# Optimization experiments

Hardware: AMD Instinct MI355X
Metric: run time of the kernel (lower is better)

The kernel has to match this reference:

```python
import jax, jax.numpy as jnp
import numpy as np

B, S, H, R = 32, 1024, 768, 24
ATT_EPS = 1e10
LN_EPS = 1e-12


def setup_inputs() -> dict:
    key = jax.random.key(0)
    ks = jax.random.split(key, 20)
    sc = 0.02
    inp = {
        "relation": jax.random.randint(ks[0], (B, 1), 0, R),
        "last_hidden_size": jax.random.normal(ks[1], (B, S, H), dtype=jnp.float32),
        "sub_head": jax.random.randint(ks[2], (B, 1), 0, S),
        "sub_tail": jax.random.randint(ks[3], (B, 1), 0, S),
        "attention_mask": jnp.ones((B, S), dtype=jnp.float32),
        # learned parameters
        "rel_emb": jax.random.normal(ks[4], (R, H)) * sc,
        "W_rf": jax.random.normal(ks[5], (H, H)) * sc,
        "b_rf": jnp.zeros((H,), jnp.float32),
        "gamma": jnp.ones((H,), jnp.float32),
        "beta": jnp.zeros((H,), jnp.float32),
        "W_wd": jax.random.normal(ks[6], (H, 2 * H)) * sc,
        "W_bd": jax.random.normal(ks[7], (H, 2 * H)) * sc,
        "Wq": jax.random.normal(ks[8], (H, H)) * sc,
        "bq": jnp.zeros((H,), jnp.float32),
        "Wk": jax.random.normal(ks[9], (H, H)) * sc,
        "bk": jnp.zeros((H,), jnp.float32),
        "Wv": jax.random.normal(ks[10], (H, H)) * sc,
        "bv": jnp.zeros((H,), jnp.float32),
        "W_obj": jax.random.normal(ks[11], (1, H)) * sc,
        "b_obj": jnp.zeros((1,), jnp.float32),
    }
    return inp


def reference(relation, last_hidden_size, sub_head, sub_tail, attention_mask,
              rel_emb, W_rf, b_rf, gamma, beta, W_wd, W_bd,
              Wq, bq, Wk, bk, Wv, bv, W_obj, b_obj):
    # dropout layers are identity in eval mode
    # relation feature: embedding -> linear -> ReLU6   [B,1,H]
    rel_feature = jnp.clip(rel_emb[relation] @ W_rf.T + b_rf, 0.0, 6.0)
    # subject span features via gather                 [B,1,H]
    sh = jnp.take_along_axis(last_hidden_size, sub_head[:, :, None], axis=1)
    st = jnp.take_along_axis(last_hidden_size, sub_tail[:, :, None], axis=1)
    sub_feature = (sh + st) * 0.5
    cond = jnp.concatenate([rel_feature, sub_feature], axis=-1)  # [B,1,2H]

    # conditional layer norm: per-sample affine from condition
    weight = cond @ W_wd.T + gamma  # [B,1,H]
    bias = cond @ W_bd.T + beta     # [B,1,H]
    mean = jnp.mean(last_hidden_size, axis=-1, keepdims=True)
    ctr = last_hidden_size - mean
    var = jnp.mean(ctr * ctr, axis=-1, keepdims=True)
    x = ctr / jnp.sqrt(var + LN_EPS)
    x = x * weight + bias  # [B,S,H]

    # custom attention: ReLU-activated q/k/v, additive mask bias, residual
    q = jax.nn.relu(x @ Wq.T + bq)
    k = jax.nn.relu(x @ Wk.T + bk)
    v = jax.nn.relu(x @ Wv.T + bv)
    e = jnp.einsum('bsh,bth->bst', q, k)  # [B,S,S]
    e = e - ATT_EPS * (1.0 - attention_mask[:, None, :])
    a = jax.nn.softmax(e, axis=-1)
    hidden = jnp.einsum('bst,bth->bsh', a, v) + x  # residual

    pred_obj_head = jnp.squeeze(hidden @ W_obj.T + b_obj, axis=-1)  # [B,S]
    return pred_obj_head, hidden
```

## Files before the change

### kernel.cpp

```cpp
#include <hip/hip_runtime.h>

constexpr int NB  = 32;
constexpr int NS  = 1024;
constexpr int NH  = 768;
constexpr int NH2 = 1536;
constexpr int NQKV = 2304;
constexpr int NBS = NB * NS;

typedef __bf16 bf16x8 __attribute__((ext_vector_type(8)));
typedef float  f32x4  __attribute__((ext_vector_type(4)));
typedef unsigned short u16x8 __attribute__((ext_vector_type(8)));

__device__ __forceinline__ unsigned short f2bf(float f) {
  unsigned int u = __builtin_bit_cast(unsigned int, f);
  u += 0x7FFFu + ((u >> 16) & 1u);
  return (unsigned short)(u >> 16);
}
__device__ __forceinline__ float bf2f(unsigned short h) {
  return __builtin_bit_cast(float, ((unsigned int)h) << 16);
}

#define GLDS16(g, l)                                                         \
  __builtin_amdgcn_global_load_lds(                                          \
      (__attribute__((address_space(1))) void*)(g),                          \
      (__attribute__((address_space(3))) void*)(l), 16, 0, 0)

#define SBAR()   asm volatile("s_barrier" ::: "memory")
#define WAITVM8() asm volatile("s_waitcnt vmcnt(8)" ::: "memory")
#define WAITVM0() asm volatile("s_waitcnt vmcnt(0)" ::: "memory")

__launch_bounds__(256)
__global__ void cond_pre(const int* __restrict__ relation,
                         const float* __restrict__ h,
                         const int* __restrict__ subh,
                         const int* __restrict__ subt,
                         const float* __restrict__ rel_emb,
                         float* __restrict__ reT, float* __restrict__ condT) {
  const int b = blockIdx.x, t = threadIdx.x;
  const int r = relation[b], sh = subh[b], st = subt[b];
  for (int k = t; k < NH; k += 256) {
    reT[(size_t)k * NB + b] = rel_emb[(size_t)r * NH + k];
    condT[(size_t)(NH + k) * NB + b] =
        0.5f * (h[((size_t)b * NS + sh) * NH + k] +
                h[((size_t)b * NS + st) * NH + k]);
  }
}

__launch_bounds__(256)
__global__ void cond_rf(const float* __restrict__ W_rf,
                        const float* __restrict__ b_rf,
                        const float* __restrict__ reT,
                        float* __restrict__ condT) {
  const int t = threadIdx.x;
  const int b = t & 31, jl = t >> 5;
  const int j = blockIdx.x * 8 + jl;
  const float4* w4 = (const float4*)(W_rf + (size_t)j * NH);
  const float* rT = reT + b;
  float a0 = 0.f, a1 = 0.f;
  for (int k4 = 0; k4 < NH / 4; k4++) {
    float4 w = w4[k4];
    const float* c = rT + (size_t)(k4 * 4) * NB;
    a0 += w.x * c[0] + w.y * c[NB];
    a1 += w.z * c[2 * NB] + w.w * c[3 * NB];
  }
  float acc = a0 + a1 + b_rf[j];
  condT[(size_t)j * NB + b] = fminf(fmaxf(acc, 0.0f), 6.0f);
}

__launch_bounds__(256)
__global__ void cond_wb(const float* __restrict__ W_wd,
                        const float* __restrict__ W_bd,
                        const float* __restrict__ gamma,
                        const float* __restrict__ beta,
                        const float* __restrict__ condT,
                        float* __restrict__ wt, float* __restrict__ bs) {
  __shared__ float redW[128], redB[128];
  const int t = threadIdx.x;
  const int b = t & 31, jl = (t >> 5) & 3, ks = t >> 7;
  const int j = blockIdx.x * 4 + jl;
  const float4* ww = (const float4*)(W_wd + (size_t)j * NH2 + ks * NH);
  const float4* wb = (const float4*)(W_bd + (size_t)j * NH2 + ks * NH);
  const float* cT = condT + (size_t)ks * NH * NB + b;
  float aw0 = 0.f, aw1 = 0.f, ab0 = 0.f, ab1 = 0.f;
  for (int k4 = 0; k4 < NH / 4; k4++) {
    float4 w = ww[k4];
    float4 v = wb[k4];
    const float* c = cT + (size_t)(k4 * 4) * NB;
    float c0 = c[0], c1 = c[NB], c2 = c[2 * NB], c3 = c[3 * NB];
    aw0 += w.x * c0 + w.y * c1;
    aw1 += w.z * c2 + w.w * c3;
    ab0 += v.x * c0 + v.y * c1;
    ab1 += v.z * c2 + v.w * c3;
  }
  float aw = aw0 + aw1, ab = ab0 + ab1;
  if (ks == 1) {
    redW[t - 128] = aw;
    redB[t - 128] = ab;
  }
  __syncthreads();
  if (ks == 0) {
    aw += redW[t];
    ab += redB[t];
    wt[(size_t)b * NH + j] = aw + gamma[j];
    bs[(size_t)b * NH + j] = ab + beta[j];
  }
}

__launch_bounds__(64)
__global__ void ln_kernel(const float* __restrict__ h,
                          const float* __restrict__ wt,
                          const float* __restrict__ bs,
                          unsigned short* __restrict__ xbf) {
  const int row = blockIdx.x;
  const int b = row >> 10;
  const int lane = threadIdx.x;
  const float4* hr = (const float4*)(h + (size_t)row * NH);
  float4 v0 = hr[lane], v1 = hr[lane + 64], v2 = hr[lane + 128];
  float sum = 0.f, sq = 0.f;
  {
    sum += v0.x + v0.y + v0.z + v0.w;
    sq  += v0.x * v0.x + v0.y * v0.y + v0.z * v0.z + v0.w * v0.w;
    sum += v1.x + v1.y + v1.z + v1.w;
    sq  += v1.x * v1.x + v1.y * v1.y + v1.z * v1.z + v1.w * v1.w;
    sum += v2.x + v2.y + v2.z + v2.w;
    sq  += v2.x * v2.x + v2.y * v2.y + v2.z * v2.z + v2.w * v2.w;
  }
  for (int off = 32; off > 0; off >>= 1) {
    sum += __shfl_xor(sum, off, 64);
    sq  += __shfl_xor(sq, off, 64);
  }
  const float mean = sum * (1.0f / NH);
  const float var  = sq * (1.0f / NH) - mean * mean;
  const float rstd = rsqrtf(var + 1e-12f);
  const float4* wr = (const float4*)(wt + (size_t)b * NH);
  const float4* br = (const float4*)(bs + (size_t)b * NH);
  ushort4* xr = (ushort4*)(xbf + (size_t)row * NH);
#pragma unroll
  for (int i = 0; i < 3; i++) {
    float4 v = (i == 0) ? v0 : (i == 1) ? v1 : v2;
    float4 w = wr[lane + 64 * i];
    float4 bb = br[lane + 64 * i];
    ushort4 o;
    o.x = f2bf((v.x - mean) * rstd * w.x + bb.x);
    o.y = f2bf((v.y - mean) * rstd * w.y + bb.y);
    o.z = f2bf((v.z - mean) * rstd * w.z + bb.z);
    o.w = f2bf((v.w - mean) * rstd * w.w + bb.w);
    xr[lane + 64 * i] = o;
  }
}

__launch_bounds__(256)
__global__ void prep_w(const float* __restrict__ Wq, const float* __restrict__ bq,
                       const float* __restrict__ Wk, const float* __restrict__ bk,
                       const float* __restrict__ Wv, const float* __restrict__ bv,
                       unsigned short* __restrict__ Wcat, float* __restrict__ bcat) {
  const int row = blockIdx.x;
  const float* Wsrc;
  const float* bsrc;
  int r;
  if (row < NH) { Wsrc = Wq; bsrc = bq; r = row; }
  else if (row < NH2) { Wsrc = Wk; bsrc = bk; r = row - NH; }
  else { Wsrc = Wv; bsrc = bv; r = row - NH2; }
  for (int j = threadIdx.x; j < NH; j += 256)
    Wcat[(size_t)row * NH + j] = f2bf(Wsrc[(size_t)r * NH + j]);
  if (threadIdx.x == 0) bcat[row] = bsrc[r];
}

template <int OUT_BF16, int RELU, int HASBIAS, int RES>
__launch_bounds__(512, 2)
__global__ void gemm256(const unsigned short* __restrict__ A, long long sAz, int lda,
                        const unsigned short* __restrict__ Bm, long long sBz, int ldb,
                        void* __restrict__ C, long long sCz, int ldc,
                        const float* __restrict__ bias,
                        const unsigned short* __restrict__ Res, long long sRz, int ldr,
                        int K, int doswz) {
  extern __shared__ char lds[];
  const int t = threadIdx.x;
  const int z = blockIdx.z;
  int id = blockIdx.x + blockIdx.y * gridDim.x;
  if (doswz) {
    const int cpx = (gridDim.x * gridDim.y) >> 3;
    id = (id & 7) * cpx + (id >> 3);
  }
  const int tileN = (id % gridDim.x) * 256;
  const int tileM = (id / gridDim.x) * 256;
  const unsigned short* Ab = A + (size_t)z * sAz + (size_t)tileM * lda;
  const unsigned short* Bb = Bm + (size_t)z * sBz + (size_t)tileN * ldb;

  const int lane = t & 63;
  const int w = t >> 6;
  const int wm = w >> 2, wn = w & 3;
  const int lr = lane & 15, hi = lane >> 4;
  const int swz = (lane & 7) << 4;
  char* myA = lds + wm * 16384;
  char* myB = lds + 65536 + (wn >> 1) * 16384;
  const int rb0 = (wn & 1) * 64;

  const int sr = t >> 3;
  const int scc = (t & 7) ^ (sr & 7);

#define STAGE(Gb, ld, dst)                                                  \
  do {                                                                      \
    _Pragma("unroll") for (int hl_ = 0; hl_ < 4; hl_++) {                   \
      GLDS16((Gb) + (size_t)(hl_ * 64 + sr) * (ld) + scc * 8,               \
             (dst) + hl_ * 8192 + (size_t)t * 16);                          \
    }                                                                       \
  } while (0)

  f32x4 acc[8][4];
#pragma unroll
  for (int m = 0; m < 8; m++)
#pragma unroll
    for (int n = 0; n < 4; n++) acc[m][n] = (f32x4)0.0f;

  const int NT = K >> 6;

  STAGE(Ab, lda, lds);
  STAGE(Bb, ldb, lds + 65536);
  STAGE(Ab + 64, lda, lds + 32768);
  STAGE(Bb + 64, ldb, lds + 65536 + 32768);
  WAITVM8();
  SBAR();

  for (int kt = 0; kt < NT; kt++) {
    const int bb = kt & 1;
    const char* Ah = myA + bb * 32768;
    const char* Bh = myB + bb * 32768;
#pragma unroll
    for (int ks = 0; ks < 2; ks++) {
      const int cb = (ks * 64 + hi * 16) ^ swz;
      bf16x8 af[8], bfr[4];
#pragma unroll
      for (int m = 0; m < 8; m++)
        af[m] = *(const bf16x8*)(Ah + (m * 16 + lr) * 128 + cb);
#pragma unroll
      for (int n = 0; n < 4; n++)
        bfr[n] = *(const bf16x8*)(Bh + (rb0 + n * 16 + lr) * 128 + cb);
      __builtin_amdgcn_s_setprio(1);
#pragma unroll
      for (int m = 0; m < 8; m++)
#pragma unroll
        for (int n = 0; n < 4; n++)
          acc[m][n] = __builtin_amdgcn_mfma_f32_16x16x32_bf16(af[m], bfr[n],
                                                              acc[m][n], 0, 0, 0);
      __builtin_amdgcn_s_setprio(0);
    }
    if (kt == NT - 1) break;
    SBAR();
    if (kt + 2 < NT) {
      STAGE(Ab + (kt + 2) * 64, lda, lds + bb * 32768);
      STAGE(Bb + (kt + 2) * 64, ldb, lds + 65536 + bb * 32768);
      WAITVM8();
    } else {
      WAITVM0();
    }
    SBAR();
  }

  const int row0 = tileM + wm * 128;
  const int col0 = tileN + wn * 64;
#pragma unroll
  for (int m = 0; m < 8; m++) {
    const int rowb = row0 + m * 16 + hi * 4;
#pragma unroll
    for (int n = 0; n < 4; n++) {
      const int col = col0 + n * 16 + lr;
      const float bv = HASBIAS ? bias[col] : 0.0f;
      f32x4 v = acc[m][n];
#pragma unroll
      for (int r = 0; r < 4; r++) {
        float x = v[r] + bv;
        if (RELU) x = fmaxf(x, 0.0f);
        if (RES)
          x += bf2f(Res[(size_t)z * sRz + (size_t)(rowb + r) * ldr + col]);
        if (OUT_BF16)
          ((unsigned short*)C)[(size_t)z * sCz + (size_t)(rowb + r) * ldc + col] =
              f2bf(x);
        else
          ((float*)C)[(size_t)z * sCz + (size_t)(rowb + r) * ldc + col] = x;
      }
    }
  }
#undef STAGE
}

__launch_bounds__(256)
__global__ void softmax_kernel(float* __restrict__ e,
                               const float* __restrict__ mask, int b0) {
  const int ri = blockIdx.x;
  const int lb = blockIdx.y;
  const int b = b0 + lb;
  float* row = e + ((size_t)lb * NS + ri) * NS;
  const int t = threadIdx.x;
  float4 v = ((const float4*)row)[t];
  float4 m = ((const float4*)(mask + (size_t)b * NS))[t];
  v.x -= 1e10f * (1.0f - m.x);
  v.y -= 1e10f * (1.0f - m.y);
  v.z -= 1e10f * (1.0f - m.z);
  v.w -= 1e10f * (1.0f - m.w);
  float mx = fmaxf(fmaxf(v.x, v.y), fmaxf(v.z, v.w));
  __shared__ float red[4];
  for (int off = 32; off > 0; off >>= 1) mx = fmaxf(mx, __shfl_xor(mx, off, 64));
  if ((t & 63) == 0) red[t >> 6] = mx;
  __syncthreads();
  mx = fmaxf(fmaxf(red[0], red[1]), fmaxf(red[2], red[3]));
  const float e0 = __expf(v.x - mx), e1 = __expf(v.y - mx);
  const float e2 = __expf(v.z - mx), e3 = __expf(v.w - mx);
  float sm = e0 + e1 + e2 + e3;
  __syncthreads();
  for (int off = 32; off > 0; off >>= 1) sm += __shfl_xor(sm, off, 64);
  if ((t & 63) == 0) red[t >> 6] = sm;
  __syncthreads();
  sm = red[0] + red[1] + red[2] + red[3];
  const float inv = 1.0f / sm;
  ushort4 o;
  o.x = f2bf(e0 * inv);
  o.y = f2bf(e1 * inv);
  o.z = f2bf(e2 * inv);
  o.w = f2bf(e3 * inv);
  ((ushort4*)row)[t] = o;
}

__launch_bounds__(256)
__global__ void transpose_v(const unsigned short* __restrict__ qkv,
                            unsigned short* __restrict__ vT) {
  const int b = blockIdx.z;
  const int s0 = blockIdx.x * 64;
  const int h0 = blockIdx.y * 64;
  __shared__ unsigned short tile[64][72];
  const int t = threadIdx.x;
  const int tx = t & 7, ty = t >> 3;
  const unsigned short* src = qkv + ((size_t)(b * NS + s0)) * NQKV + NH2 + h0;
#pragma unroll
  for (int i = 0; i < 2; i++) {
    const int s = ty + 32 * i;
    u16x8 vv = *(const u16x8*)(src + (size_t)s * NQKV + tx * 8);
#pragma unroll
    for (int j = 0; j < 8; j++) tile[s][tx * 8 + j] = vv[j];
  }
  __syncthreads();
  unsigned short* dst = vT + ((size_t)b * NH + h0) * NS + s0;
#pragma unroll
  for (int i = 0; i < 2; i++) {
    const int hh = ty + 32 * i;
    u16x8 o;
#pragma unroll
    for (int j = 0; j < 8; j++) o[j] = tile[tx * 8 + j][hh];
    *(u16x8*)(dst + (size_t)hh * NS + tx * 8) = o;
  }
}

__launch_bounds__(64)
__global__ void pred_kernel(const float* __restrict__ hidden,
                            const float* __restrict__ wobj,
                            const float* __restrict__ bobj,
                            float* __restrict__ pred) {
  const int row = blockIdx.x;
  const int lane = threadIdx.x;
  const float4* hr = (const float4*)(hidden + (size_t)row * NH);
  const float4* wr = (const float4*)wobj;
  float s = 0.f;
#pragma unroll
  for (int i = 0; i < 3; i++) {
    float4 a = hr[lane + 64 * i];
    float4 w = wr[lane + 64 * i];
    s += a.x * w.x + a.y * w.y + a.z * w.z + a.w * w.w;
  }
  for (int off = 32; off > 0; off >>= 1) s += __shfl_xor(s, off, 64);
  if (lane == 0) pred[row] = s + bobj[0];
}

extern "C" void kernel_launch(void* const* d_in, const int* in_sizes, int n_in,
                              void* d_out, int out_size, void* d_ws,
                              size_t ws_size, hipStream_t stream) {
  const int* relation   = (const int*)d_in[0];
  const float* lhs      = (const float*)d_in[1];
  const int* sub_head   = (const int*)d_in[2];
  const int* sub_tail   = (const int*)d_in[3];
  const float* att_mask = (const float*)d_in[4];
  const float* rel_emb  = (const float*)d_in[5];
  const float* W_rf     = (const float*)d_in[6];
  const float* b_rf     = (const float*)d_in[7];
  const float* gamma    = (const float*)d_in[8];
  const float* beta     = (const float*)d_in[9];
  const float* W_wd     = (const float*)d_in[10];
  const float* W_bd     = (const float*)d_in[11];
  const float* Wq       = (const float*)d_in[12];
  const float* bq       = (const float*)d_in[13];
  const float* Wk       = (const float*)d_in[14];
  const float* bk       = (const float*)d_in[15];
  const float* Wv       = (const float*)d_in[16];
  const float* bv       = (const float*)d_in[17];
  const float* W_obj    = (const float*)d_in[18];
  const float* b_obj    = (const float*)d_in[19];

  char* ws = (char*)d_ws;
  unsigned short* Wcat = (unsigned short*)(ws + 0);
  float* bcat  = (float*)(ws + 3538944);
  float* wt    = (float*)(ws + 3548160);
  float* bs    = (float*)(ws + 3646464);
  float* reT   = (float*)(ws + 3744768);
  float* condT = (float*)(ws + 3843072);
  unsigned short* xbf = (unsigned short*)(ws + 4039680);
  unsigned short* qkv = (unsigned short*)(ws + 54371328);
  unsigned short* vT  = (unsigned short*)(ws + 205366272);
  float* ebuf = (float*)(ws + 255697920);

  float* out_pred = (float*)d_out;
  float* out_hidden = out_pred + NBS;

  const size_t fixed = 255697920ull;
  size_t avail = ws_size > fixed ? ws_size - fixed : 0;
  int CB = 32;
  while (CB > 1 && (size_t)CB * (size_t)NS * NS * 4 > avail) CB >>= 1;

  prep_w<<<dim3(NQKV), dim3(256), 0, stream>>>(Wq, bq, Wk, bk, Wv, bv, Wcat, bcat);
  cond_pre<<<dim3(NB), dim3(256), 0, stream>>>(relation, lhs, sub_head, sub_tail,
                                               rel_emb, reT, condT);
  cond_rf<<<dim3(NH / 8), dim3(256), 0, stream>>>(W_rf, b_rf, reT, condT);
  cond_wb<<<dim3(NH / 4), dim3(256), 0, stream>>>(W_wd, W_bd, gamma, beta, condT,
                                                  wt, bs);
  ln_kernel<<<dim3(NBS), dim3(64), 0, stream>>>(lhs, wt, bs, xbf);

  gemm256<1, 1, 1, 0><<<dim3(NQKV / 256, NBS / 256, 1), dim3(512), 131072, stream>>>(
      xbf, 0, NH, Wcat, 0, NH, qkv, 0, NQKV, bcat, nullptr, 0, 0, NH, 1);

  transpose_v<<<dim3(NS / 64, NH / 64, NB), dim3(256), 0, stream>>>(qkv, vT);

  for (int b0 = 0; b0 < NB; b0 += CB) {
    gemm256<0, 0, 0, 0><<<dim3(NS / 256, NS / 256, CB), dim3(512), 131072, stream>>>(
        qkv + (size_t)b0 * NS * NQKV, (long long)NS * NQKV, NQKV,
        qkv + (size_t)b0 * NS * NQKV + NH, (long long)NS * NQKV, NQKV,
        ebuf, (long long)NS * NS, NS, nullptr, nullptr, 0, 0, NH, 0);
    softmax_kernel<<<dim3(NS, CB), dim3(256), 0, stream>>>(ebuf, att_mask, b0);
    gemm256<0, 0, 0, 1><<<dim3(NH / 256, NS / 256, CB), dim3(512), 131072, stream>>>(
        (const unsigned short*)ebuf, (long long)NS * 2048, 2048,
        vT + (size_t)b0 * NH * NS, (long long)NH * NS, NS,
        out_hidden + (size_t)b0 * NS * NH, (long long)NS * NH, NH, nullptr,
        xbf + (size_t)b0 * NS * NH, (long long)NS * NH, NH, NS, 0);
  }

  pred_kernel<<<dim3(NBS), dim3(64), 0, stream>>>(out_hidden, W_obj, b_obj,
                                                  out_pred);
}
```

Baseline: 515.3 us.

## Restructure GEMM main loop into four-quadrant interleaved LDS-read/MFMA/prefetch schedule

Replaces the two-tile-ahead prefetch with a single-tile-ahead double buffer. The per-iteration MFMA work is split into four 4x2 quadrants, and LDS fragment reads and global-to-LDS staging are interleaved with barriers and explicit lgkmcnt waits between quadrants. The aim is to overlap LDS reads and global loads with MFMA execution and to cut register pressure from holding all fragments at once. In exchange it adds many more barriers per iteration and shortens the prefetch distance, which may expose global memory latency.

```diff
diff --git a/kernel.cpp b/kernel.cpp
--- a/kernel.cpp
+++ b/kernel.cpp
@@ -25,9 +25,13 @@
       (__attribute__((address_space(1))) void*)(g),                          \
       (__attribute__((address_space(3))) void*)(l), 16, 0, 0)
 
-#define SBAR()   asm volatile("s_barrier" ::: "memory")
-#define WAITVM8() asm volatile("s_waitcnt vmcnt(8)" ::: "memory")
+#define SBAR()    asm volatile("s_barrier" ::: "memory")
 #define WAITVM0() asm volatile("s_waitcnt vmcnt(0)" ::: "memory")
+#define LGKM0()                                                              \
+  do {                                                                       \
+    asm volatile("s_waitcnt lgkmcnt(0)" ::: "memory");                       \
+    __builtin_amdgcn_sched_barrier(0);                                       \
+  } while (0)
 
 __launch_bounds__(256)
 __global__ void cond_pre(const int* __restrict__ relation,
@@ -192,14 +196,12 @@
   const int wm = w >> 2, wn = w & 3;
   const int lr = lane & 15, hi = lane >> 4;
   const int swz = (lane & 7) << 4;
-  char* myA = lds + wm * 16384;
-  char* myB = lds + 65536 + (wn >> 1) * 16384;
   const int rb0 = (wn & 1) * 64;
 
   const int sr = t >> 3;
   const int scc = (t & 7) ^ (sr & 7);
 
-#define STAGE(Gb, ld, dst)                                                  \
+#define STAGE4(Gb, ld, dst)                                                 \
   do {                                                                      \
     _Pragma("unroll") for (int hl_ = 0; hl_ < 4; hl_++) {                   \
       GLDS16((Gb) + (size_t)(hl_ * 64 + sr) * (ld) + scc * 8,               \
@@ -207,6 +209,33 @@
     }                                                                       \
   } while (0)
 
+#define RD_A(m0)                                                            \
+  do {                                                                      \
+    _Pragma("unroll") for (int mm_ = 0; mm_ < 4; mm_++)                     \
+      _Pragma("unroll") for (int ks_ = 0; ks_ < 2; ks_++)                   \
+        aF[mm_][ks_] = *(const bf16x8*)(Ah + ((m0) * 16 + mm_ * 16 + lr) * 128 + \
+                                        ((ks_ * 64 + hi * 16) ^ swz));      \
+  } while (0)
+
+#define RD_B(n0)                                                            \
+  do {                                                                      \
+    _Pragma("unroll") for (int nn_ = 0; nn_ < 2; nn_++)                     \
+      _Pragma("unroll") for (int ks_ = 0; ks_ < 2; ks_++)                   \
+        bF[nn_][ks_] = *(const bf16x8*)(Bh + (rb0 + (n0) * 16 + nn_ * 16 + lr) * 128 + \
+                                        ((ks_ * 64 + hi * 16) ^ swz));      \
+  } while (0)
+
+#define MFMA_Q(m0, n0)                                                      \
+  do {                                                                      \
+    __builtin_amdgcn_s_setprio(1);                                          \
+    _Pragma("unroll") for (int ks_ = 0; ks_ < 2; ks_++)                     \
+      _Pragma("unroll") for (int mm_ = 0; mm_ < 4; mm_++)                   \
+        _Pragma("unroll") for (int nn_ = 0; nn_ < 2; nn_++)                 \
+          acc[(m0) + mm_][(n0) + nn_] = __builtin_amdgcn_mfma_f32_16x16x32_bf16( \
+              aF[mm_][ks_], bF[nn_][ks_], acc[(m0) + mm_][(n0) + nn_], 0, 0, 0); \
+    __builtin_amdgcn_s_setprio(0);                                          \
+  } while (0)
+
   f32x4 acc[8][4];
 #pragma unroll
   for (int m = 0; m < 8; m++)
@@ -215,45 +244,45 @@
 
   const int NT = K >> 6;
 
-  STAGE(Ab, lda, lds);
-  STAGE(Bb, ldb, lds + 65536);
-  STAGE(Ab + 64, lda, lds + 32768);
-  STAGE(Bb + 64, ldb, lds + 65536 + 32768);
-  WAITVM8();
+  STAGE4(Ab, lda, lds);
+  STAGE4(Bb, ldb, lds + 65536);
+  WAITVM0();
   SBAR();
 
   for (int kt = 0; kt < NT; kt++) {
     const int bb = kt & 1;
-    const char* Ah = myA + bb * 32768;
-    const char* Bh = myB + bb * 32768;
-#pragma unroll
-    for (int ks = 0; ks < 2; ks++) {
-      const int cb = (ks * 64 + hi * 16) ^ swz;
-      bf16x8 af[8], bfr[4];
-#pragma unroll
-      for (int m = 0; m < 8; m++)
-        af[m] = *(const bf16x8*)(Ah + (m * 16 + lr) * 128 + cb);
-#pragma unroll
-      for (int n = 0; n < 4; n++)
-        bfr[n] = *(const bf16x8*)(Bh + (rb0 + n * 16 + lr) * 128 + cb);
-      __builtin_amdgcn_s_setprio(1);
-#pragma unroll
-      for (int m = 0; m < 8; m++)
-#pragma unroll
-        for (int n = 0; n < 4; n++)
-          acc[m][n] = __builtin_amdgcn_mfma_f32_16x16x32_bf16(af[m], bfr[n],
-                                                              acc[m][n], 0, 0, 0);
-      __builtin_amdgcn_s_setprio(0);
-    }
-    if (kt == NT - 1) break;
-    SBAR();
-    if (kt + 2 < NT) {
-      STAGE(Ab + (kt + 2) * 64, lda, lds + bb * 32768);
-      STAGE(Bb + (kt + 2) * 64, ldb, lds + 65536 + bb * 32768);
-      WAITVM8();
-    } else {
-      WAITVM0();
-    }
+    const char* Ah = lds + bb * 32768 + wm * 16384;
+    const char* Bh = lds + 65536 + bb * 32768 + (wn >> 1) * 16384;
+    const int stg = (kt + 1 < NT);
+    bf16x8 aF[4][2], bF[2][2];
+
+    RD_A(0);
+    RD_B(0);
+    if (stg) STAGE4(Ab + (size_t)(kt + 1) * 64, lda, lds + (bb ^ 1) * 32768);
+    SBAR();
+    LGKM0();
+    MFMA_Q(0, 0);
+    SBAR();
+
+    RD_B(2);
+    if (stg)
+      STAGE4(Bb + (size_t)(kt + 1) * 64, ldb, lds + 65536 + (bb ^ 1) * 32768);
+    SBAR();
+    LGKM0();
+    MFMA_Q(0, 2);
+    SBAR();
+
+    RD_A(4);
+    SBAR();
+    LGKM0();
+    MFMA_Q(4, 2);
+    SBAR();
+
+    RD_B(0);
+    SBAR();
+    LGKM0();
+    MFMA_Q(4, 0);
+    if (stg) WAITVM0();
     SBAR();
   }
 
@@ -281,7 +310,10 @@
       }
     }
   }
-#undef STAGE
+#undef STAGE4
+#undef RD_A
+#undef RD_B
+#undef MFMA_Q
 }
 
 __launch_bounds__(256)
```

Measured after the change: 503.5 us. 2.3% less time.

## Restructure GEMM mainloop to triple-buffered 32-wide K tiles with single barrier

Applied to the files above, without the earlier changes.

Rewrites the 256x256 bf16 GEMM mainloop to use K-steps of 32 with a three-stage LDS ring buffer (96 KB instead of 128 KB). Prefetch for tile kt+2 is issued before computing tile kt, and only one barrier per iteration remains. The LDS reads are interleaved with MFMA quadrants so fragment loads overlap compute, using a new XOR swizzle for the 64-byte rows. The intent is to hide global-load latency and cut barrier stalls, at the cost of twice as many loop iterations and a more intricate swizzle that must stay bank-conflict free.

```diff
diff --git a/kernel.cpp b/kernel.cpp
--- a/kernel.cpp
+++ b/kernel.cpp
@@ -25,8 +25,8 @@
       (__attribute__((address_space(1))) void*)(g),                          \
       (__attribute__((address_space(3))) void*)(l), 16, 0, 0)
 
-#define SBAR()   asm volatile("s_barrier" ::: "memory")
-#define WAITVM8() asm volatile("s_waitcnt vmcnt(8)" ::: "memory")
+#define SBAR()    asm volatile("s_barrier" ::: "memory")
+#define WAITVM4() asm volatile("s_waitcnt vmcnt(4)" ::: "memory")
 #define WAITVM0() asm volatile("s_waitcnt vmcnt(0)" ::: "memory")
 
 __launch_bounds__(256)
@@ -191,70 +191,78 @@
   const int w = t >> 6;
   const int wm = w >> 2, wn = w & 3;
   const int lr = lane & 15, hi = lane >> 4;
-  const int swz = (lane & 7) << 4;
-  char* myA = lds + wm * 16384;
-  char* myB = lds + 65536 + (wn >> 1) * 16384;
-  const int rb0 = (wn & 1) * 64;
-
-  const int sr = t >> 3;
-  const int scc = (t & 7) ^ (sr & 7);
-
-#define STAGE(Gb, ld, dst)                                                  \
+  const int rsw = ((lr >> 1) & 3) << 4;
+  const int cbyte = (hi << 4) ^ rsw;
+
+  const int sgc = (t & 3) ^ ((t >> 3) & 3);
+
+#define STAGEOP(Gb, ld, dst)                                                \
   do {                                                                      \
-    _Pragma("unroll") for (int hl_ = 0; hl_ < 4; hl_++) {                   \
-      GLDS16((Gb) + (size_t)(hl_ * 64 + sr) * (ld) + scc * 8,               \
+    _Pragma("unroll") for (int hl_ = 0; hl_ < 2; hl_++) {                   \
+      GLDS16((Gb) + (size_t)(hl_ * 128 + (t >> 2)) * (ld) + sgc * 8,        \
              (dst) + hl_ * 8192 + (size_t)t * 16);                          \
     }                                                                       \
   } while (0)
 
+#define RD_A(dst, m0, Ahp)                                                  \
+  do {                                                                      \
+    _Pragma("unroll") for (int mm_ = 0; mm_ < 4; mm_++)                     \
+      dst[mm_] = *(const bf16x8*)((Ahp) + (wm * 128 + (m0) * 16 + mm_ * 16 + lr) * 64 + cbyte); \
+  } while (0)
+
+#define RD_B(dst, n0, Bhp)                                                  \
+  do {                                                                      \
+    _Pragma("unroll") for (int nn_ = 0; nn_ < 2; nn_++)                     \
+      dst[nn_] = *(const bf16x8*)((Bhp) + (wn * 64 + (n0) * 16 + nn_ * 16 + lr) * 64 + cbyte); \
+  } while (0)
+
+#define MFMA_Q(m0, n0, av, bv)                                              \
+  do {                                                                      \
+    __builtin_amdgcn_s_setprio(1);                                          \
+    _Pragma("unroll") for (int mm_ = 0; mm_ < 4; mm_++)                     \
+      _Pragma("unroll") for (int nn_ = 0; nn_ < 2; nn_++)                   \
+        acc[(m0) + mm_][(n0) + nn_] = __builtin_amdgcn_mfma_f32_16x16x32_bf16( \
+            av[mm_], bv[nn_], acc[(m0) + mm_][(n0) + nn_], 0, 0, 0);        \
+    __builtin_amdgcn_s_setprio(0);                                          \
+  } while (0)
+
   f32x4 acc[8][4];
 #pragma unroll
   for (int m = 0; m < 8; m++)
 #pragma unroll
     for (int n = 0; n < 4; n++) acc[m][n] = (f32x4)0.0f;
 
-  const int NT = K >> 6;
-
-  STAGE(Ab, lda, lds);
-  STAGE(Bb, ldb, lds + 65536);
-  STAGE(Ab + 64, lda, lds + 32768);
-  STAGE(Bb + 64, ldb, lds + 65536 + 32768);
-  WAITVM8();
+  const int NT = K >> 5;
+
+  STAGEOP(Ab, lda, lds);
+  STAGEOP(Bb, ldb, lds + 16384);
+  STAGEOP(Ab + 32, lda, lds + 32768);
+  STAGEOP(Bb + 32, ldb, lds + 32768 + 16384);
+  WAITVM4();
   SBAR();
 
+  int cb = 0, sb = 2;
   for (int kt = 0; kt < NT; kt++) {
-    const int bb = kt & 1;
-    const char* Ah = myA + bb * 32768;
-    const char* Bh = myB + bb * 32768;
-#pragma unroll
-    for (int ks = 0; ks < 2; ks++) {
-      const int cb = (ks * 64 + hi * 16) ^ swz;
-      bf16x8 af[8], bfr[4];
-#pragma unroll
-      for (int m = 0; m < 8; m++)
-        af[m] = *(const bf16x8*)(Ah + (m * 16 + lr) * 128 + cb);
-#pragma unroll
-      for (int n = 0; n < 4; n++)
-        bfr[n] = *(const bf16x8*)(Bh + (rb0 + n * 16 + lr) * 128 + cb);
-      __builtin_amdgcn_s_setprio(1);
-#pragma unroll
-      for (int m = 0; m < 8; m++)
-#pragma unroll
-        for (int n = 0; n < 4; n++)
-          acc[m][n] = __builtin_amdgcn_mfma_f32_16x16x32_bf16(af[m], bfr[n],
-                                                              acc[m][n], 0, 0, 0);
-      __builtin_amdgcn_s_setprio(0);
+    const char* Ah = lds + cb * 32768;
+    const char* Bh = Ah + 16384;
+    if (kt + 2 < NT) {
+      STAGEOP(Ab + (size_t)(kt + 2) * 32, lda, lds + sb * 32768);
+      STAGEOP(Bb + (size_t)(kt + 2) * 32, ldb, lds + sb * 32768 + 16384);
     }
+    bf16x8 a0[4], a4[4], b0[2], b2[2];
+    RD_A(a0, 0, Ah);
+    RD_B(b0, 0, Bh);
+    MFMA_Q(0, 0, a0, b0);
+    RD_B(b2, 2, Bh);
+    MFMA_Q(0, 2, a0, b2);
+    RD_A(a4, 4, Ah);
+    MFMA_Q(4, 2, a4, b2);
+    MFMA_Q(4, 0, a4, b0);
     if (kt == NT - 1) break;
+    if (kt == NT - 2) WAITVM0(); else WAITVM4();
     SBAR();
-    if (kt + 2 < NT) {
-      STAGE(Ab + (kt + 2) * 64, lda, lds + bb * 32768);
-      STAGE(Bb + (kt + 2) * 64, ldb, lds + 65536 + bb * 32768);
-      WAITVM8();
-    } else {
-      WAITVM0();
-    }
-    SBAR();
+    cb = (cb == 2) ? 0 : cb + 1;
+    sb = (sb == 2) ? 0 : sb + 1;
   }
 
   const int row0 = tileM + wm * 128;
@@ -281,7 +289,10 @@
       }
     }
   }
-#undef STAGE
+#undef STAGEOP
+#undef RD_A
+#undef RD_B
+#undef MFMA_Q
 }
 
 __launch_bounds__(256)
@@ -422,18 +433,18 @@
                                                   wt, bs);
   ln_kernel<<<dim3(NBS), dim3(64), 0, stream>>>(lhs, wt, bs, xbf);
 
-  gemm256<1, 1, 1, 0><<<dim3(NQKV / 256, NBS / 256, 1), dim3(512), 131072, stream>>>(
+  gemm256<1, 1, 1, 0><<<dim3(NQKV / 256, NBS / 256, 1), dim3(512), 98304, stream>>>(
       xbf, 0, NH, Wcat, 0, NH, qkv, 0, NQKV, bcat, nullptr, 0, 0, NH, 1);
 
   transpose_v<<<dim3(NS / 64, NH / 64, NB), dim3(256), 0, stream>>>(qkv, vT);
 
   for (int b0 = 0; b0 < NB; b0 += CB) {
-    gemm256<0, 0, 0, 0><<<dim3(NS / 256, NS / 256, CB), dim3(512), 131072, stream>>>(
+    gemm256<0, 0, 0, 0><<<dim3(NS / 256, NS / 256, CB), dim3(512), 98304, stream>>>(
         qkv + (size_t)b0 * NS * NQKV, (long long)NS * NQKV, NQKV,
         qkv + (size_t)b0 * NS * NQKV + NH, (long long)NS * NQKV, NQKV,
         ebuf, (long long)NS * NS, NS, nullptr, nullptr, 0, 0, NH, 0);
     softmax_kernel<<<dim3(NS, CB), dim3(256), 0, stream>>>(ebuf, att_mask, b0);
-    gemm256<0, 0, 0, 1><<<dim3(NH / 256, NS / 256, CB), dim3(512), 131072, stream>>>(
+    gemm256<0, 0, 0, 1><<<dim3(NH / 256, NS / 256, CB), dim3(512), 98304, stream>>>(
         (const unsigned short*)ebuf, (long long)NS * 2048, 2048,
         vT + (size_t)b0 * NH * NS, (long long)NH * NS, NS,
         out_hidden + (size_t)b0 * NS * NH, (long long)NS * NH, NH, nullptr,
```

New measurement: 511.4 us. No clear change (-0.8%).
